# Kernel optimization log

Hardware: AMD Instinct MI355X
Metric: run time of the kernel (lower is better)

Reference implementation:

```python
import jax, jax.numpy as jnp
import numpy as np

E = 16        # n_routed_experts
K = 2         # n_activated_experts (top-k)
DIM = 1024    # model dim
INTER = 704   # moe_inter_dim
B, S = 4, 1024


def setup_inputs() -> dict:
    key = jax.random.key(0)
    ks = jax.random.split(key, 5)
    x = jax.random.normal(ks[0], (B, S, DIM), dtype=jnp.float32)
    Wg = jax.random.normal(ks[1], (E, DIM), dtype=jnp.float32) * 0.02   # gate (Linear, no bias)
    W1 = jax.random.normal(ks[2], (E, DIM, INTER), dtype=jnp.float32) * 0.02
    W3 = jax.random.normal(ks[3], (E, DIM, INTER), dtype=jnp.float32) * 0.02
    W2 = jax.random.normal(ks[4], (E, INTER, DIM), dtype=jnp.float32) * 0.02
    return {"x": x, "Wg": Wg, "W1": W1, "W2": W2, "W3": W3}


def reference(x, Wg, W1, W2, W3):
    # Single-process semantics of MoEWithAll2All: the all2all dispatch/combine is
    # pure communication; the math is: softmax router -> top-k -> renormalize ->
    # per-expert SwiGLU MLP on routed tokens -> weighted combine at original slots.
    Bb, Ss, D = x.shape
    xf = x.reshape(-1, D)                              # [N, D], N = B*S
    logits = xf @ Wg.T                                 # [N, E]
    probs = jax.nn.softmax(logits, axis=-1)
    topw, topi = jax.lax.top_k(probs, K)               # [N, K]
    topw = topw / topw.sum(axis=-1, keepdims=True)
    # gates[n, e] = routed weight of token n for expert e (0 if not routed):
    # identical math to the masked gather/scatter dispatch in the original.
    gates = (jax.nn.one_hot(topi, E, dtype=xf.dtype) * topw[..., None]).sum(axis=1)  # [N, E]
    out = jnp.zeros_like(xf)
    for e in range(E):                                 # small fixed loop over experts
        h = jax.nn.silu(xf @ W1[e]) * (xf @ W3[e])     # SwiGLU expert, [N, INTER]
        out = out + gates[:, e:e + 1] * (h @ W2[e])    # combine with gate weights
    return out.reshape(Bb, Ss, D)
```

## Files before the change

### kernel.cpp

```cpp
#include <hip/hip_runtime.h>

#define NTOK 4096
#define DDIM 1024
#define IDIM 704
#define NEXP 16
#define NSLOT 8192
#define MAXT 128
#define RTRBLK 512

typedef __attribute__((ext_vector_type(8))) short bf16x8;
typedef __attribute__((ext_vector_type(4))) float f32x4;
typedef __attribute__((ext_vector_type(4))) unsigned short us4;
typedef __attribute__((ext_vector_type(2))) unsigned int u32x2;

__device__ __forceinline__ unsigned short f2bf(float f) {
  union { float f; unsigned int u; } v; v.f = f;
  unsigned int r = v.u + 0x7fffu + ((v.u >> 16) & 1u);
  return (unsigned short)(r >> 16);
}

__device__ __forceinline__ float bf2f(unsigned short b) {
  union { unsigned int u; float f; } v; v.u = ((unsigned int)b) << 16;
  return v.f;
}

__device__ __forceinline__ unsigned int cvt_pk_bf16(float a, float b) {
  unsigned int r;
  asm("v_cvt_pk_bf16_f32 %0, %1, %2" : "=v"(r) : "v"(a), "v"(b));
  return r;
}

__device__ __forceinline__ void gload_lds16(const void* g, void* l) {
  __builtin_amdgcn_global_load_lds((const __attribute__((address_space(1))) void*)g,
                                   (__attribute__((address_space(3))) void*)l, 16, 0, 0);
}

__device__ __forceinline__ void load_b(const float* wt, int ns, bool ok, f32x4* v) {
#pragma unroll
  for (int j = 0; j < 4; ++j)
    v[j] = ok ? *(const f32x4*)(wt + (size_t)j * ns) : (f32x4)0.f;
}

__device__ __forceinline__ void write_b(const f32x4* v, unsigned short* buf, int kk, int nq) {
  int h8 = (kk & 1) * 8;
  int phys = (kk >> 1) ^ (nq & 3);
#pragma unroll
  for (int c = 0; c < 4; ++c) {
    int row = nq * 4 + c;
    u32x2 o = { cvt_pk_bf16(v[0][c], v[1][c]), cvt_pk_bf16(v[2][c], v[3][c]) };
    *(u32x2*)((char*)buf + row * 64 + phys * 16 + h8) = o;
  }
}

__global__ __launch_bounds__(256, 4)
void k_front(const float* __restrict__ x, const float* __restrict__ Wg,
             int* __restrict__ tok_e, float* __restrict__ tok_w,
             unsigned short* __restrict__ Xb) {
  int b = blockIdx.x;
  int lane = threadIdx.x & 63;
  int wv = threadIdx.x >> 6;
  int tk0 = b * 8 + wv * 2;
  f32x4 xv[2][4];
#pragma unroll
  for (int tok = 0; tok < 2; ++tok) {
    const f32x4* xr = (const f32x4*)(x + (size_t)(tk0 + tok) * DDIM);
    us4* xbr = (us4*)(Xb + (size_t)(tk0 + tok) * DDIM);
#pragma unroll
    for (int c = 0; c < 4; ++c) {
      xv[tok][c] = xr[c * 64 + lane];
      us4 o;
#pragma unroll
      for (int j = 0; j < 4; ++j) o[j] = f2bf(xv[tok][c][j]);
      xbr[c * 64 + lane] = o;
    }
  }
  float p[2][NEXP];
#pragma unroll
  for (int e = 0; e < NEXP; ++e) {
    const f32x4* wr = (const f32x4*)(Wg + (size_t)e * DDIM);
    float s0 = 0.f, s1 = 0.f;
#pragma unroll
    for (int c = 0; c < 4; ++c) {
      f32x4 w4 = wr[c * 64 + lane];
      s0 += xv[0][c][0]*w4[0] + xv[0][c][1]*w4[1] + xv[0][c][2]*w4[2] + xv[0][c][3]*w4[3];
      s1 += xv[1][c][0]*w4[0] + xv[1][c][1]*w4[1] + xv[1][c][2]*w4[2] + xv[1][c][3]*w4[3];
    }
    p[0][e] = s0; p[1][e] = s1;
  }
#pragma unroll
  for (int off = 32; off >= 1; off >>= 1)
#pragma unroll
    for (int e = 0; e < NEXP; ++e) {
      p[0][e] += __shfl_xor(p[0][e], off);
      p[1][e] += __shfl_xor(p[1][e], off);
    }
#pragma unroll
  for (int tok = 0; tok < 2; ++tok) {
    int i0 = 0; float b0 = p[tok][0];
#pragma unroll
    for (int e = 1; e < NEXP; ++e) if (p[tok][e] > b0) { b0 = p[tok][e]; i0 = e; }
    int i1 = -1; float b1 = -3.4e38f;
#pragma unroll
    for (int e = 0; e < NEXP; ++e) if (e != i0 && p[tok][e] > b1) { b1 = p[tok][e]; i1 = e; }
    if (lane == 0) {
      int tk = tk0 + tok;
      float w0 = 1.f / (1.f + __expf(b1 - b0));
      tok_e[2*tk] = i0; tok_e[2*tk+1] = i1;
      tok_w[2*tk] = w0; tok_w[2*tk+1] = 1.f - w0;
    }
  }
}

__global__ void k_scan_scatter(const int* __restrict__ tok_e, const float* __restrict__ tok_w,
                               int* __restrict__ counts, int* __restrict__ offsets,
                               int* __restrict__ ntiles, int* __restrict__ tile_e,
                               int* __restrict__ tile_m0, int* __restrict__ token_map,
                               float* __restrict__ gate_w, int* __restrict__ slot_of) {
  int eb = blockIdx.x;
  int t = threadIdx.x, lane = t & 63, wv = t >> 6;
  __shared__ unsigned long long masks[4][32];
  __shared__ int wcnt[4][NEXP];
  __shared__ int counts_s[NEXP];
  int ce[NEXP];
#pragma unroll
  for (int e = 0; e < NEXP; ++e) ce[e] = 0;
  int base = wv * 2048 + lane;
  int te = tok_e[base];
#pragma unroll 1
  for (int s = 0; s < 32; ++s) {
    int ten = (s < 31) ? tok_e[base + (s + 1) * 64] : 0;
    unsigned long long B0 = __ballot(te & 1);
    unsigned long long B1 = __ballot(te & 2);
    unsigned long long B2 = __ballot(te & 4);
    unsigned long long B3 = __ballot(te & 8);
#pragma unroll
    for (int e = 0; e < NEXP; ++e) {
      unsigned long long m = ((e & 1) ? B0 : ~B0) & ((e & 2) ? B1 : ~B1) &
                             ((e & 4) ? B2 : ~B2) & ((e & 8) ? B3 : ~B3);
      ce[e] += (int)__popcll(m);
      if (e == eb && lane == 0) masks[wv][s] = m;
    }
    te = ten;
  }
  if (lane == 0) {
#pragma unroll
    for (int e = 0; e < NEXP; ++e) wcnt[wv][e] = ce[e];
  }
  __syncthreads();
  if (t < NEXP) {
    int s = wcnt[0][t] + wcnt[1][t] + wcnt[2][t] + wcnt[3][t];
    counts_s[t] = s;
    if (eb == 0) counts[t] = s;
  }
  __syncthreads();
  if (eb == 0 && t == 0) {
    int acc = 0, nt = 0;
    for (int e = 0; e < NEXP; ++e) {
      offsets[e] = acc;
      int cc = counts_s[e];
      for (int m0 = 0; m0 < cc; m0 += 128) { tile_e[nt] = e; tile_m0[nt] = m0; ++nt; }
      acc += cc;
    }
    offsets[NEXP] = acc;
    *ntiles = nt;
  }
  int run = 0;
  for (int e = 0; e < eb; ++e) run += counts_s[e];
  for (int w = 0; w < wv; ++w) run += wcnt[w][eb];
  unsigned long long below = (lane == 63) ? 0x7fffffffffffffffull : ((1ull << lane) - 1ull);
#pragma unroll 1
  for (int s = 0; s < 32; ++s) {
    unsigned long long m = masks[wv][s];
    if ((m >> lane) & 1ull) {
      int i = wv * 2048 + s * 64 + lane;
      int slot = run + (int)__popcll(m & below);
      token_map[slot] = i >> 1;
      gate_w[slot] = tok_w[i];
      slot_of[i] = slot;
    }
    run += (int)__popcll(m);
  }
}

__global__ __launch_bounds__(256, 2)
void k_gemm1(const unsigned short* __restrict__ Xb, const float* __restrict__ W1,
             const float* __restrict__ W3, const int* __restrict__ token_map,
             const float* __restrict__ gate_w, const int* __restrict__ ntiles,
             const int* __restrict__ tile_e, const int* __restrict__ tile_m0,
             const int* __restrict__ offsets, const int* __restrict__ counts,
             unsigned short* __restrict__ H) {
  int idx = blockIdx.x;
  int xcd = idx & 7, r = idx >> 3;
  int g = (r >> 2) * 8 + xcd;
  int mm = r & 3;
  int ty = (g / 6) * 4 + mm;
  if (ty >= *ntiles) return;
  int n0 = (g % 6) * 128;
  int e = tile_e[ty], m0 = tile_m0[ty];
  int base_slot = offsets[e] + m0;
  int cnt = counts[e] - m0; if (cnt > 128) cnt = 128;

  __shared__ unsigned short As[2][128 * 32];
  __shared__ unsigned short B1s[2][128 * 32];
  __shared__ unsigned short B3s[2][128 * 32];

  int t = threadIdx.x;
  int arow = t >> 2, kc = (t & 3) * 8;
  int r0i = base_slot + arow;      if (r0i > NSLOT - 1) r0i = NSLOT - 1;
  int r1i = base_slot + 64 + arow; if (r1i > NSLOT - 1) r1i = NSLOT - 1;
  const unsigned short* ag0 = Xb + (size_t)token_map[r0i] * DDIM + kc;
  const unsigned short* ag1 = Xb + (size_t)token_map[r1i] * DDIM + kc;
  int d0 = t * 8, d1 = 2048 + t * 8;

  int kk = t >> 5, nq = t & 31;
  bool bok = (n0 + nq * 4 + 4) <= IDIM;
  const float* w1t = W1 + (size_t)e * DDIM * IDIM + (size_t)(kk * 4) * IDIM + (n0 + nq * 4);
  const float* w3t = W3 + (size_t)e * DDIM * IDIM + (size_t)(kk * 4) * IDIM + (n0 + nq * 4);

  int lane = t & 63, wv = t >> 6;
  int wm = (wv >> 1) * 64, wn = (wv & 1) * 64;
  int lm = lane & 15, kg = lane >> 4;
  int ao[4], bo[4];
#pragma unroll
  for (int i = 0; i < 4; ++i) {
    ao[i] = (wm + i * 16 + lm) * 32 + kg * 8;
    int brow = wn + i * 16 + lm;
    bo[i] = brow * 64 + ((kg ^ ((brow >> 2) & 3)) << 4);
  }

  f32x4 acc1[4][4], acc3[4][4];
#pragma unroll
  for (int i = 0; i < 4; ++i)
#pragma unroll
    for (int j = 0; j < 4; ++j) { acc1[i][j] = 0.f; acc3[i][j] = 0.f; }

  {
    gload_lds16(ag0, As[0] + d0);
    gload_lds16(ag1, As[0] + d1);
    f32x4 b1r[4], b3r[4];
    load_b(w1t, IDIM, bok, b1r);
    load_b(w3t, IDIM, bok, b3r);
    write_b(b1r, B1s[0], kk, nq);
    write_b(b3r, B3s[0], kk, nq);
  }

  for (int k0 = 0; k0 < DDIM; k0 += 32) {
    int cur = (k0 >> 5) & 1, nx = cur ^ 1;
    __syncthreads();
    f32x4 b1r[4], b3r[4];
    bool more = (k0 + 32) < DDIM;
    if (more) {
      int kn = k0 + 32;
      gload_lds16(ag0 + kn, As[nx] + d0);
      gload_lds16(ag1 + kn, As[nx] + d1);
      load_b(w1t + (size_t)kn * IDIM, IDIM, bok, b1r);
      load_b(w3t + (size_t)kn * IDIM, IDIM, bok, b3r);
    }
    bf16x8 av[4], b1v[4], b3v[4];
#pragma unroll
    for (int i = 0; i < 4; ++i) {
      av[i]  = *(const bf16x8*)(As[cur] + ao[i]);
      b1v[i] = *(const bf16x8*)((const char*)B1s[cur] + bo[i]);
      b3v[i] = *(const bf16x8*)((const char*)B3s[cur] + bo[i]);
    }
#pragma unroll
    for (int mi = 0; mi < 4; ++mi)
#pragma unroll
      for (int ni = 0; ni < 4; ++ni) {
        acc1[mi][ni] = __builtin_amdgcn_mfma_f32_16x16x32_bf16(av[mi], b1v[ni], acc1[mi][ni], 0, 0, 0);
        acc3[mi][ni] = __builtin_amdgcn_mfma_f32_16x16x32_bf16(av[mi], b3v[ni], acc3[mi][ni], 0, 0, 0);
      }
    if (more) {
      write_b(b1r, B1s[nx], kk, nq);
      write_b(b3r, B3s[nx], kk, nq);
    }
  }

#pragma unroll
  for (int mi = 0; mi < 4; ++mi)
#pragma unroll
    for (int rr = 0; rr < 4; ++rr) {
      int orow = wm + mi * 16 + kg * 4 + rr;
      if (orow < cnt) {
        int slot = base_slot + orow;
        float gw = gate_w[slot];
        unsigned short* hrow = H + (size_t)slot * IDIM;
#pragma unroll
        for (int ni = 0; ni < 4; ++ni) {
          int nn = n0 + wn + ni * 16 + lm;
          if (nn < IDIM) {
            float v1 = acc1[mi][ni][rr];
            float v3 = acc3[mi][ni][rr];
            float hh = v1 / (1.f + __expf(-v1)) * v3 * gw;
            hrow[nn] = f2bf(hh);
          }
        }
      }
    }
}

__global__ __launch_bounds__(256, 3)
void k_gemm2(const unsigned short* __restrict__ H, const float* __restrict__ W2,
             const int* __restrict__ ntiles, const int* __restrict__ tile_e,
             const int* __restrict__ tile_m0, const int* __restrict__ offsets,
             const int* __restrict__ counts, unsigned short* __restrict__ O2) {
  int idx = blockIdx.x;
  int xcd = idx & 7, r = idx >> 3;
  int g = (r >> 2) * 8 + xcd;
  int mm = r & 3;
  int ty = (g >> 3) * 4 + mm;
  if (ty >= *ntiles) return;
  int n0 = (g & 7) * 128;
  int e = tile_e[ty], m0 = tile_m0[ty];
  int base_slot = offsets[e] + m0;
  int cnt = counts[e] - m0; if (cnt > 128) cnt = 128;

  __shared__ unsigned short As[2][128 * 32];
  __shared__ unsigned short Bs[2][128 * 32];

  int t = threadIdx.x;
  int arow = t >> 2, kc = (t & 3) * 8;
  int r0i = base_slot + arow;      if (r0i > NSLOT - 1) r0i = NSLOT - 1;
  int r1i = base_slot + 64 + arow; if (r1i > NSLOT - 1) r1i = NSLOT - 1;
  const unsigned short* ag0 = H + (size_t)r0i * IDIM + kc;
  const unsigned short* ag1 = H + (size_t)r1i * IDIM + kc;
  int d0 = t * 8, d1 = 2048 + t * 8;

  int kk = t >> 5, nq = t & 31;
  const float* w2t = W2 + (size_t)e * IDIM * DDIM + (size_t)(kk * 4) * DDIM + (n0 + nq * 4);

  int lane = t & 63, wv = t >> 6;
  int wm = (wv >> 1) * 64, wn = (wv & 1) * 64;
  int lm = lane & 15, kg = lane >> 4;
  int ao[4], bo[4];
#pragma unroll
  for (int i = 0; i < 4; ++i) {
    ao[i] = (wm + i * 16 + lm) * 32 + kg * 8;
    int brow = wn + i * 16 + lm;
    bo[i] = brow * 64 + ((kg ^ ((brow >> 2) & 3)) << 4);
  }

  f32x4 acc[4][4];
#pragma unroll
  for (int i = 0; i < 4; ++i)
#pragma unroll
    for (int j = 0; j < 4; ++j) acc[i][j] = 0.f;

  {
    gload_lds16(ag0, As[0] + d0);
    gload_lds16(ag1, As[0] + d1);
    f32x4 br[4];
    load_b(w2t, DDIM, true, br);
    write_b(br, Bs[0], kk, nq);
  }

  for (int k0 = 0; k0 < IDIM; k0 += 32) {
    int cur = (k0 >> 5) & 1, nx = cur ^ 1;
    __syncthreads();
    f32x4 br[4];
    bool more = (k0 + 32) < IDIM;
    if (more) {
      int kn = k0 + 32;
      gload_lds16(ag0 + kn, As[nx] + d0);
      gload_lds16(ag1 + kn, As[nx] + d1);
      load_b(w2t + (size_t)kn * DDIM, DDIM, true, br);
    }
    bf16x8 av[4], bv[4];
#pragma unroll
    for (int i = 0; i < 4; ++i) {
      av[i] = *(const bf16x8*)(As[cur] + ao[i]);
      bv[i] = *(const bf16x8*)((const char*)Bs[cur] + bo[i]);
    }
#pragma unroll
    for (int mi = 0; mi < 4; ++mi)
#pragma unroll
      for (int ni = 0; ni < 4; ++ni)
        acc[mi][ni] = __builtin_amdgcn_mfma_f32_16x16x32_bf16(av[mi], bv[ni], acc[mi][ni], 0, 0, 0);
    if (more) write_b(br, Bs[nx], kk, nq);
  }

#pragma unroll
  for (int mi = 0; mi < 4; ++mi)
#pragma unroll
    for (int rr = 0; rr < 4; ++rr) {
      int orow = wm + mi * 16 + kg * 4 + rr;
      if (orow < cnt) {
        unsigned short* op = O2 + (size_t)(base_slot + orow) * DDIM + n0;
#pragma unroll
        for (int ni = 0; ni < 4; ++ni)
          op[wn + ni * 16 + lm] = f2bf(acc[mi][ni][rr]);
      }
    }
}

__global__ void k_combine(const unsigned short* __restrict__ O2, const int* __restrict__ slot_of,
                          float* __restrict__ out) {
  int tk = blockIdx.x, tt = threadIdx.x;
  int s0 = slot_of[2 * tk], s1 = slot_of[2 * tk + 1];
  us4 a = ((const us4*)(O2 + (size_t)s0 * DDIM))[tt];
  us4 b = ((const us4*)(O2 + (size_t)s1 * DDIM))[tt];
  f32x4 o;
#pragma unroll
  for (int j = 0; j < 4; ++j) o[j] = bf2f(a[j]) + bf2f(b[j]);
  ((f32x4*)(out + (size_t)tk * DDIM))[tt] = o;
}

extern "C" void kernel_launch(void* const* d_in, const int* in_sizes, int n_in,
                              void* d_out, int out_size, void* d_ws, size_t ws_size,
                              hipStream_t stream) {
  const float* x  = (const float*)d_in[0];
  const float* Wg = (const float*)d_in[1];
  const float* W1 = (const float*)d_in[2];
  const float* W2 = (const float*)d_in[3];
  const float* W3 = (const float*)d_in[4];
  float* out = (float*)d_out;

  char* ws = (char*)d_ws;
  size_t off = 0;
  unsigned short* Xb = (unsigned short*)(ws + off); off += (size_t)NTOK * DDIM * 2;
  unsigned short* H  = (unsigned short*)(ws + off); off += (size_t)NSLOT * IDIM * 2;
  unsigned short* O2 = (unsigned short*)(ws + off); off += (size_t)NSLOT * DDIM * 2;
  int* counts  = (int*)(ws + off); off += 64;
  int* offsets = (int*)(ws + off); off += 128;
  int* ntiles  = (int*)(ws + off); off += 64;
  int* tile_e  = (int*)(ws + off); off += MAXT * 4;
  int* tile_m0 = (int*)(ws + off); off += MAXT * 4;
  int* tok_e   = (int*)(ws + off); off += NSLOT * 4;
  float* tok_w = (float*)(ws + off); off += NSLOT * 4;
  int* token_map = (int*)(ws + off); off += NSLOT * 4;
  float* gate_w  = (float*)(ws + off); off += NSLOT * 4;
  int* slot_of   = (int*)(ws + off); off += NSLOT * 4;

  k_front<<<RTRBLK, 256, 0, stream>>>(x, Wg, tok_e, tok_w, Xb);
  k_scan_scatter<<<NEXP, 256, 0, stream>>>(tok_e, tok_w, counts, offsets, ntiles,
                                           tile_e, tile_m0, token_map, gate_w, slot_of);
  k_gemm1<<<480, 256, 0, stream>>>(Xb, W1, W3, token_map, gate_w, ntiles, tile_e,
                                   tile_m0, offsets, counts, H);
  k_gemm2<<<640, 256, 0, stream>>>(H, W2, ntiles, tile_e, tile_m0, offsets, counts, O2);
  k_combine<<<4096, 256, 0, stream>>>(O2, slot_of, out);
}
```

Measured before the change: 318.3 us.

## Halve GEMM N-tile to 64 and split weight loading across thread halves

Both expert GEMMs switch from 128x128 to 128x64 output tiles, with each wave taking a 32-row strip. This roughly doubles the grid (880 and 1280 blocks) and raises the occupancy hints. In gemm1, half the threads load W1 and the other half W3, which removes the per-thread dual weight load and the bounds check, since 704 is a multiple of 64. The B-tile LDS writes also rotate their column order per thread to reduce bank conflicts. The trade-off is that the A tile is reloaded for twice as many N-tiles, raising gathered activation traffic, and only half the threads load weights in gemm2.

```diff
diff --git a/kernel.cpp b/kernel.cpp
--- a/kernel.cpp
+++ b/kernel.cpp
@@ -35,17 +35,18 @@
                                    (__attribute__((address_space(3))) void*)l, 16, 0, 0);
 }
 
-__device__ __forceinline__ void load_b(const float* wt, int ns, bool ok, f32x4* v) {
+__device__ __forceinline__ void load_b(const float* wt, int ns, f32x4* v) {
 #pragma unroll
   for (int j = 0; j < 4; ++j)
-    v[j] = ok ? *(const f32x4*)(wt + (size_t)j * ns) : (f32x4)0.f;
+    v[j] = *(const f32x4*)(wt + (size_t)j * ns);
 }
 
 __device__ __forceinline__ void write_b(const f32x4* v, unsigned short* buf, int kk, int nq) {
   int h8 = (kk & 1) * 8;
-  int phys = (kk >> 1) ^ (nq & 3);
-#pragma unroll
-  for (int c = 0; c < 4; ++c) {
+  int phys = ((kk >> 1) ^ nq) & 3;
+#pragma unroll
+  for (int cc = 0; cc < 4; ++cc) {
+    int c = (cc + nq) & 3;
     int row = nq * 4 + c;
     u32x2 o = { cvt_pk_bf16(v[0][c], v[1][c]), cvt_pk_bf16(v[2][c], v[3][c]) };
     *(u32x2*)((char*)buf + row * 64 + phys * 16 + h8) = o;
@@ -182,27 +183,25 @@
   }
 }
 
-__global__ __launch_bounds__(256, 2)
+__global__ __launch_bounds__(256, 3)
 void k_gemm1(const unsigned short* __restrict__ Xb, const float* __restrict__ W1,
              const float* __restrict__ W3, const int* __restrict__ token_map,
              const float* __restrict__ gate_w, const int* __restrict__ ntiles,
              const int* __restrict__ tile_e, const int* __restrict__ tile_m0,
              const int* __restrict__ offsets, const int* __restrict__ counts,
              unsigned short* __restrict__ H) {
-  int idx = blockIdx.x;
-  int xcd = idx & 7, r = idx >> 3;
-  int g = (r >> 2) * 8 + xcd;
-  int mm = r & 3;
-  int ty = (g / 6) * 4 + mm;
+  int wg = blockIdx.x;
+  int g = (wg & 7) * 110 + (wg >> 3);
+  int ty = g / 11, nb = g % 11;
   if (ty >= *ntiles) return;
-  int n0 = (g % 6) * 128;
+  int n0 = nb * 64;
   int e = tile_e[ty], m0 = tile_m0[ty];
   int base_slot = offsets[e] + m0;
   int cnt = counts[e] - m0; if (cnt > 128) cnt = 128;
 
   __shared__ unsigned short As[2][128 * 32];
-  __shared__ unsigned short B1s[2][128 * 32];
-  __shared__ unsigned short B3s[2][128 * 32];
+  __shared__ unsigned short B1s[2][64 * 32];
+  __shared__ unsigned short B3s[2][64 * 32];
 
   int t = threadIdx.x;
   int arow = t >> 2, kc = (t & 3) * 8;
@@ -212,111 +211,103 @@
   const unsigned short* ag1 = Xb + (size_t)token_map[r1i] * DDIM + kc;
   int d0 = t * 8, d1 = 2048 + t * 8;
 
-  int kk = t >> 5, nq = t & 31;
-  bool bok = (n0 + nq * 4 + 4) <= IDIM;
-  const float* w1t = W1 + (size_t)e * DDIM * IDIM + (size_t)(kk * 4) * IDIM + (n0 + nq * 4);
-  const float* w3t = W3 + (size_t)e * DDIM * IDIM + (size_t)(kk * 4) * IDIM + (n0 + nq * 4);
+  int bmat = t >> 7;
+  int bt = t & 127;
+  int nq = bt & 15, kk = bt >> 4;
+  const float* wsrc = (bmat ? W3 : W1) + (size_t)e * DDIM * IDIM
+                      + (size_t)(kk * 4) * IDIM + (n0 + nq * 4);
+  unsigned short (*Bst)[64 * 32] = bmat ? B3s : B1s;
 
   int lane = t & 63, wv = t >> 6;
-  int wm = (wv >> 1) * 64, wn = (wv & 1) * 64;
+  int wm = wv * 32;
   int lm = lane & 15, kg = lane >> 4;
-  int ao[4], bo[4];
+  int ao[2], bo[4];
+#pragma unroll
+  for (int i = 0; i < 2; ++i) ao[i] = (wm + i * 16 + lm) * 32 + kg * 8;
 #pragma unroll
   for (int i = 0; i < 4; ++i) {
-    ao[i] = (wm + i * 16 + lm) * 32 + kg * 8;
-    int brow = wn + i * 16 + lm;
+    int brow = i * 16 + lm;
     bo[i] = brow * 64 + ((kg ^ ((brow >> 2) & 3)) << 4);
   }
 
-  f32x4 acc1[4][4], acc3[4][4];
-#pragma unroll
-  for (int i = 0; i < 4; ++i)
+  f32x4 acc1[2][4], acc3[2][4];
+#pragma unroll
+  for (int i = 0; i < 2; ++i)
 #pragma unroll
     for (int j = 0; j < 4; ++j) { acc1[i][j] = 0.f; acc3[i][j] = 0.f; }
 
+  f32x4 br[4];
   {
     gload_lds16(ag0, As[0] + d0);
     gload_lds16(ag1, As[0] + d1);
-    f32x4 b1r[4], b3r[4];
-    load_b(w1t, IDIM, bok, b1r);
-    load_b(w3t, IDIM, bok, b3r);
-    write_b(b1r, B1s[0], kk, nq);
-    write_b(b3r, B3s[0], kk, nq);
+    load_b(wsrc, IDIM, br);
+    write_b(br, Bst[0], kk, nq);
   }
 
   for (int k0 = 0; k0 < DDIM; k0 += 32) {
     int cur = (k0 >> 5) & 1, nx = cur ^ 1;
     __syncthreads();
-    f32x4 b1r[4], b3r[4];
     bool more = (k0 + 32) < DDIM;
     if (more) {
       int kn = k0 + 32;
       gload_lds16(ag0 + kn, As[nx] + d0);
       gload_lds16(ag1 + kn, As[nx] + d1);
-      load_b(w1t + (size_t)kn * IDIM, IDIM, bok, b1r);
-      load_b(w3t + (size_t)kn * IDIM, IDIM, bok, b3r);
-    }
-    bf16x8 av[4], b1v[4], b3v[4];
+      load_b(wsrc + (size_t)kn * IDIM, IDIM, br);
+    }
+    bf16x8 av[2], b1v[4], b3v[4];
+#pragma unroll
+    for (int i = 0; i < 2; ++i) av[i] = *(const bf16x8*)(As[cur] + ao[i]);
 #pragma unroll
     for (int i = 0; i < 4; ++i) {
-      av[i]  = *(const bf16x8*)(As[cur] + ao[i]);
       b1v[i] = *(const bf16x8*)((const char*)B1s[cur] + bo[i]);
       b3v[i] = *(const bf16x8*)((const char*)B3s[cur] + bo[i]);
     }
 #pragma unroll
-    for (int mi = 0; mi < 4; ++mi)
+    for (int mi = 0; mi < 2; ++mi)
 #pragma unroll
       for (int ni = 0; ni < 4; ++ni) {
         acc1[mi][ni] = __builtin_amdgcn_mfma_f32_16x16x32_bf16(av[mi], b1v[ni], acc1[mi][ni], 0, 0, 0);
         acc3[mi][ni] = __builtin_amdgcn_mfma_f32_16x16x32_bf16(av[mi], b3v[ni], acc3[mi][ni], 0, 0, 0);
       }
-    if (more) {
-      write_b(b1r, B1s[nx], kk, nq);
-      write_b(b3r, B3s[nx], kk, nq);
-    }
-  }
-
-#pragma unroll
-  for (int mi = 0; mi < 4; ++mi)
+    if (more) write_b(br, Bst[nx], kk, nq);
+  }
+
+#pragma unroll
+  for (int mi = 0; mi < 2; ++mi)
 #pragma unroll
     for (int rr = 0; rr < 4; ++rr) {
       int orow = wm + mi * 16 + kg * 4 + rr;
       if (orow < cnt) {
         int slot = base_slot + orow;
         float gw = gate_w[slot];
-        unsigned short* hrow = H + (size_t)slot * IDIM;
+        unsigned short* hrow = H + (size_t)slot * IDIM + n0;
 #pragma unroll
         for (int ni = 0; ni < 4; ++ni) {
-          int nn = n0 + wn + ni * 16 + lm;
-          if (nn < IDIM) {
-            float v1 = acc1[mi][ni][rr];
-            float v3 = acc3[mi][ni][rr];
-            float hh = v1 / (1.f + __expf(-v1)) * v3 * gw;
-            hrow[nn] = f2bf(hh);
-          }
+          float v1 = acc1[mi][ni][rr];
+          float v3 = acc3[mi][ni][rr];
+          float hh = v1 / (1.f + __expf(-v1)) * v3 * gw;
+          hrow[ni * 16 + lm] = f2bf(hh);
         }
       }
     }
 }
 
-__global__ __launch_bounds__(256, 3)
+__global__ __launch_bounds__(256, 4)
 void k_gemm2(const unsigned short* __restrict__ H, const float* __restrict__ W2,
              const int* __restrict__ ntiles, const int* __restrict__ tile_e,
              const int* __restrict__ tile_m0, const int* __restrict__ offsets,
              const int* __restrict__ counts, unsigned short* __restrict__ O2) {
-  int idx = blockIdx.x;
-  int xcd = idx & 7, r = idx >> 3;
-  int g = (r >> 2) * 8 + xcd;
-  int mm = r & 3;
-  int ty = (g >> 3) * 4 + mm;
+  int wg = blockIdx.x;
+  int g = (wg & 7) * 160 + (wg >> 3);
+  int ty = g >> 4, nb = g & 15;
   if (ty >= *ntiles) return;
-  int n0 = (g & 7) * 128;
+  int n0 = nb * 64;
   int e = tile_e[ty], m0 = tile_m0[ty];
   int base_slot = offsets[e] + m0;
   int cnt = counts[e] - m0; if (cnt > 128) cnt = 128;
 
   __shared__ unsigned short As[2][128 * 32];
-  __shared__ unsigned short Bs[2][128 * 32];
+  __shared__ unsigned short Bs[2][64 * 32];
 
   int t = threadIdx.x;
   int arow = t >> 2, kc = (t & 3) * 8;
@@ -326,61 +317,63 @@
   const unsigned short* ag1 = H + (size_t)r1i * IDIM + kc;
   int d0 = t * 8, d1 = 2048 + t * 8;
 
-  int kk = t >> 5, nq = t & 31;
-  const float* w2t = W2 + (size_t)e * IDIM * DDIM + (size_t)(kk * 4) * DDIM + (n0 + nq * 4);
+  int bt = t & 127;
+  int nq = bt & 15, kk = bt >> 4;
+  const float* wsrc = W2 + (size_t)e * IDIM * DDIM + (size_t)(kk * 4) * DDIM + (n0 + nq * 4);
 
   int lane = t & 63, wv = t >> 6;
-  int wm = (wv >> 1) * 64, wn = (wv & 1) * 64;
+  int wm = wv * 32;
   int lm = lane & 15, kg = lane >> 4;
-  int ao[4], bo[4];
+  int ao[2], bo[4];
+#pragma unroll
+  for (int i = 0; i < 2; ++i) ao[i] = (wm + i * 16 + lm) * 32 + kg * 8;
 #pragma unroll
   for (int i = 0; i < 4; ++i) {
-    ao[i] = (wm + i * 16 + lm) * 32 + kg * 8;
-    int brow = wn + i * 16 + lm;
+    int brow = i * 16 + lm;
     bo[i] = brow * 64 + ((kg ^ ((brow >> 2) & 3)) << 4);
   }
 
-  f32x4 acc[4][4];
-#pragma unroll
-  for (int i = 0; i < 4; ++i)
+  f32x4 acc[2][4];
+#pragma unroll
+  for (int i = 0; i < 2; ++i)
 #pragma unroll
     for (int j = 0; j < 4; ++j) acc[i][j] = 0.f;
 
+  f32x4 br[4];
   {
     gload_lds16(ag0, As[0] + d0);
     gload_lds16(ag1, As[0] + d1);
-    f32x4 br[4];
-    load_b(w2t, DDIM, true, br);
-    write_b(br, Bs[0], kk, nq);
+    if (t < 128) {
+      load_b(wsrc, DDIM, br);
+      write_b(br, Bs[0], kk, nq);
+    }
   }
 
   for (int k0 = 0; k0 < IDIM; k0 += 32) {
     int cur = (k0 >> 5) & 1, nx = cur ^ 1;
     __syncthreads();
-    f32x4 br[4];
     bool more = (k0 + 32) < IDIM;
     if (more) {
       int kn = k0 + 32;
       gload_lds16(ag0 + kn, As[nx] + d0);
       gload_lds16(ag1 + kn, As[nx] + d1);
-      load_b(w2t + (size_t)kn * DDIM, DDIM, true, br);
-    }
-    bf16x8 av[4], bv[4];
-#pragma unroll
-    for (int i = 0; i < 4; ++i) {
-      av[i] = *(const bf16x8*)(As[cur] + ao[i]);
-      bv[i] = *(const bf16x8*)((const char*)Bs[cur] + bo[i]);
-    }
-#pragma unroll
-    for (int mi = 0; mi < 4; ++mi)
+      if (t < 128) load_b(wsrc + (size_t)kn * DDIM, DDIM, br);
+    }
+    bf16x8 av[2], bv[4];
+#pragma unroll
+    for (int i = 0; i < 2; ++i) av[i] = *(const bf16x8*)(As[cur] + ao[i]);
+#pragma unroll
+    for (int i = 0; i < 4; ++i) bv[i] = *(const bf16x8*)((const char*)Bs[cur] + bo[i]);
+#pragma unroll
+    for (int mi = 0; mi < 2; ++mi)
 #pragma unroll
       for (int ni = 0; ni < 4; ++ni)
         acc[mi][ni] = __builtin_amdgcn_mfma_f32_16x16x32_bf16(av[mi], bv[ni], acc[mi][ni], 0, 0, 0);
-    if (more) write_b(br, Bs[nx], kk, nq);
-  }
-
-#pragma unroll
-  for (int mi = 0; mi < 4; ++mi)
+    if (more && t < 128) write_b(br, Bs[nx], kk, nq);
+  }
+
+#pragma unroll
+  for (int mi = 0; mi < 2; ++mi)
 #pragma unroll
     for (int rr = 0; rr < 4; ++rr) {
       int orow = wm + mi * 16 + kg * 4 + rr;
@@ -388,7 +381,7 @@
         unsigned short* op = O2 + (size_t)(base_slot + orow) * DDIM + n0;
 #pragma unroll
         for (int ni = 0; ni < 4; ++ni)
-          op[wn + ni * 16 + lm] = f2bf(acc[mi][ni][rr]);
+          op[ni * 16 + lm] = f2bf(acc[mi][ni][rr]);
       }
     }
 }
@@ -434,8 +427,8 @@
   k_front<<<RTRBLK, 256, 0, stream>>>(x, Wg, tok_e, tok_w, Xb);
   k_scan_scatter<<<NEXP, 256, 0, stream>>>(tok_e, tok_w, counts, offsets, ntiles,
                                            tile_e, tile_m0, token_map, gate_w, slot_of);
-  k_gemm1<<<480, 256, 0, stream>>>(Xb, W1, W3, token_map, gate_w, ntiles, tile_e,
+  k_gemm1<<<880, 256, 0, stream>>>(Xb, W1, W3, token_map, gate_w, ntiles, tile_e,
                                    tile_m0, offsets, counts, H);
-  k_gemm2<<<640, 256, 0, stream>>>(H, W2, ntiles, tile_e, tile_m0, offsets, counts, O2);
+  k_gemm2<<<1280, 256, 0, stream>>>(H, W2, ntiles, tile_e, tile_m0, offsets, counts, O2);
   k_combine<<<4096, 256, 0, stream>>>(O2, slot_of, out);
 }
```

Measured after the change: 488.5 us. 1.53x slower.

## Pre-transpose W2 to bf16 inside gemm1 grid and use direct LDS loads in gemm2

Applied to the files above, without the earlier changes.

Adds extra blocks to the gemm1 launch that convert W2 from fp32 [I,D] to a bf16 transposed [D,I] workspace buffer through a swizzled LDS tile. gemm2 then loads its B operand with global_load_lds like the A operand, dropping the per-iteration fp32 register loads, conversion and LDS writes. It also rotates the store order in write_b to reduce LDS bank conflicts. The cost is an extra full pass over W2 (read fp32, write bf16) each call, which adds work to the gemm1 launch and consumes bandwidth alongside it.

```diff
diff --git a/kernel.cpp b/kernel.cpp
--- a/kernel.cpp
+++ b/kernel.cpp
@@ -7,10 +7,13 @@
 #define NSLOT 8192
 #define MAXT 128
 #define RTRBLK 512
+#define G1BLK 480
+#define W2TBLK 1408
 
 typedef __attribute__((ext_vector_type(8))) short bf16x8;
 typedef __attribute__((ext_vector_type(4))) float f32x4;
 typedef __attribute__((ext_vector_type(4))) unsigned short us4;
+typedef __attribute__((ext_vector_type(8))) unsigned short us8;
 typedef __attribute__((ext_vector_type(2))) unsigned int u32x2;
 
 __device__ __forceinline__ unsigned short f2bf(float f) {
@@ -45,7 +48,8 @@
   int h8 = (kk & 1) * 8;
   int phys = (kk >> 1) ^ (nq & 3);
 #pragma unroll
-  for (int c = 0; c < 4; ++c) {
+  for (int cc = 0; cc < 4; ++cc) {
+    int c = (cc + nq) & 3;
     int row = nq * 4 + c;
     u32x2 o = { cvt_pk_bf16(v[0][c], v[1][c]), cvt_pk_bf16(v[2][c], v[3][c]) };
     *(u32x2*)((char*)buf + row * 64 + phys * 16 + h8) = o;
@@ -184,12 +188,55 @@
 
 __global__ __launch_bounds__(256, 2)
 void k_gemm1(const unsigned short* __restrict__ Xb, const float* __restrict__ W1,
-             const float* __restrict__ W3, const int* __restrict__ token_map,
-             const float* __restrict__ gate_w, const int* __restrict__ ntiles,
-             const int* __restrict__ tile_e, const int* __restrict__ tile_m0,
-             const int* __restrict__ offsets, const int* __restrict__ counts,
-             unsigned short* __restrict__ H) {
+             const float* __restrict__ W3, const float* __restrict__ W2src,
+             const int* __restrict__ token_map, const float* __restrict__ gate_w,
+             const int* __restrict__ ntiles, const int* __restrict__ tile_e,
+             const int* __restrict__ tile_m0, const int* __restrict__ offsets,
+             const int* __restrict__ counts, unsigned short* __restrict__ H,
+             unsigned short* __restrict__ W2T) {
+  __shared__ unsigned short As[2][128 * 32];
+  __shared__ unsigned short B1s[2][128 * 32];
+  __shared__ unsigned short B3s[2][128 * 32];
   int idx = blockIdx.x;
+  int t = threadIdx.x;
+  if (idx >= G1BLK) {
+    unsigned short (*lds)[64 * 64] = (unsigned short (*)[64 * 64])As;
+    int tb = idx - G1BLK;
+    int kx = tb % 11; int rest = tb / 11; int np = rest & 7; int e = rest >> 3;
+    const float* src = W2src + (size_t)e * IDIM * DDIM;
+    unsigned short* dst = W2T + (size_t)e * DDIM * IDIM;
+    int k0 = kx * 64;
+    int kr4 = (t >> 4) * 4, nc4 = (t & 15) * 4;
+    int n0a = np * 128, n0b = n0a + 64;
+    f32x4 v0[4], v1[4];
+#pragma unroll
+    for (int j = 0; j < 4; ++j) {
+      v0[j] = *(const f32x4*)(src + (size_t)(k0 + kr4 + j) * DDIM + n0a + nc4);
+      v1[j] = *(const f32x4*)(src + (size_t)(k0 + kr4 + j) * DDIM + n0b + nc4);
+    }
+    int c8 = kr4 >> 3, half = (kr4 >> 2) & 1;
+#pragma unroll
+    for (int i = 0; i < 4; ++i) {
+      int row = nc4 + i;
+      int addr = row * 64 + ((c8 ^ ((row >> 2) & 7)) << 3) + half * 4;
+      us4 o0 = { f2bf(v0[0][i]), f2bf(v0[1][i]), f2bf(v0[2][i]), f2bf(v0[3][i]) };
+      us4 o1 = { f2bf(v1[0][i]), f2bf(v1[1][i]), f2bf(v1[2][i]), f2bf(v1[3][i]) };
+      *(us4*)(lds[0] + addr) = o0;
+      *(us4*)(lds[1] + addr) = o1;
+    }
+    __syncthreads();
+    int nr = t >> 3, kc8 = t & 7;
+#pragma unroll
+    for (int q = 0; q < 2; ++q) {
+      int row = nr + q * 32;
+      int a = row * 64 + ((kc8 ^ ((row >> 2) & 7)) << 3);
+      us8 oA = *(const us8*)(lds[0] + a);
+      us8 oB = *(const us8*)(lds[1] + a);
+      *(us8*)(dst + (size_t)(n0a + row) * IDIM + k0 + kc8 * 8) = oA;
+      *(us8*)(dst + (size_t)(n0b + row) * IDIM + k0 + kc8 * 8) = oB;
+    }
+    return;
+  }
   int xcd = idx & 7, r = idx >> 3;
   int g = (r >> 2) * 8 + xcd;
   int mm = r & 3;
@@ -200,11 +247,6 @@
   int base_slot = offsets[e] + m0;
   int cnt = counts[e] - m0; if (cnt > 128) cnt = 128;
 
-  __shared__ unsigned short As[2][128 * 32];
-  __shared__ unsigned short B1s[2][128 * 32];
-  __shared__ unsigned short B3s[2][128 * 32];
-
-  int t = threadIdx.x;
   int arow = t >> 2, kc = (t & 3) * 8;
   int r0i = base_slot + arow;      if (r0i > NSLOT - 1) r0i = NSLOT - 1;
   int r1i = base_slot + 64 + arow; if (r1i > NSLOT - 1) r1i = NSLOT - 1;
@@ -300,7 +342,7 @@
 }
 
 __global__ __launch_bounds__(256, 3)
-void k_gemm2(const unsigned short* __restrict__ H, const float* __restrict__ W2,
+void k_gemm2(const unsigned short* __restrict__ H, const unsigned short* __restrict__ W2T,
              const int* __restrict__ ntiles, const int* __restrict__ tile_e,
              const int* __restrict__ tile_m0, const int* __restrict__ offsets,
              const int* __restrict__ counts, unsigned short* __restrict__ O2) {
@@ -319,15 +361,14 @@
   __shared__ unsigned short Bs[2][128 * 32];
 
   int t = threadIdx.x;
-  int arow = t >> 2, kc = (t & 3) * 8;
-  int r0i = base_slot + arow;      if (r0i > NSLOT - 1) r0i = NSLOT - 1;
-  int r1i = base_slot + 64 + arow; if (r1i > NSLOT - 1) r1i = NSLOT - 1;
+  int row = t >> 2, kc = (t & 3) * 8;
+  int r0i = base_slot + row;      if (r0i > NSLOT - 1) r0i = NSLOT - 1;
+  int r1i = base_slot + 64 + row; if (r1i > NSLOT - 1) r1i = NSLOT - 1;
   const unsigned short* ag0 = H + (size_t)r0i * IDIM + kc;
   const unsigned short* ag1 = H + (size_t)r1i * IDIM + kc;
+  const unsigned short* bg0 = W2T + ((size_t)e * DDIM + n0 + row) * IDIM + kc;
+  const unsigned short* bg1 = bg0 + (size_t)64 * IDIM;
   int d0 = t * 8, d1 = 2048 + t * 8;
-
-  int kk = t >> 5, nq = t & 31;
-  const float* w2t = W2 + (size_t)e * IDIM * DDIM + (size_t)(kk * 4) * DDIM + (n0 + nq * 4);
 
   int lane = t & 63, wv = t >> 6;
   int wm = (wv >> 1) * 64, wn = (wv & 1) * 64;
@@ -336,8 +377,7 @@
 #pragma unroll
   for (int i = 0; i < 4; ++i) {
     ao[i] = (wm + i * 16 + lm) * 32 + kg * 8;
-    int brow = wn + i * 16 + lm;
-    bo[i] = brow * 64 + ((kg ^ ((brow >> 2) & 3)) << 4);
+    bo[i] = (wn + i * 16 + lm) * 32 + kg * 8;
   }
 
   f32x4 acc[4][4];
@@ -346,37 +386,32 @@
 #pragma unroll
     for (int j = 0; j < 4; ++j) acc[i][j] = 0.f;
 
-  {
-    gload_lds16(ag0, As[0] + d0);
-    gload_lds16(ag1, As[0] + d1);
-    f32x4 br[4];
-    load_b(w2t, DDIM, true, br);
-    write_b(br, Bs[0], kk, nq);
-  }
+  gload_lds16(ag0, As[0] + d0);
+  gload_lds16(ag1, As[0] + d1);
+  gload_lds16(bg0, Bs[0] + d0);
+  gload_lds16(bg1, Bs[0] + d1);
 
   for (int k0 = 0; k0 < IDIM; k0 += 32) {
-    int cur = (k0 >> 5) & 1, nx = cur ^ 1;
+    int cur = (k0 >> 5) & 1;
     __syncthreads();
-    f32x4 br[4];
-    bool more = (k0 + 32) < IDIM;
-    if (more) {
-      int kn = k0 + 32;
+    if (k0 + 32 < IDIM) {
+      int nx = cur ^ 1, kn = k0 + 32;
       gload_lds16(ag0 + kn, As[nx] + d0);
       gload_lds16(ag1 + kn, As[nx] + d1);
-      load_b(w2t + (size_t)kn * DDIM, DDIM, true, br);
+      gload_lds16(bg0 + kn, Bs[nx] + d0);
+      gload_lds16(bg1 + kn, Bs[nx] + d1);
     }
     bf16x8 av[4], bv[4];
 #pragma unroll
     for (int i = 0; i < 4; ++i) {
       av[i] = *(const bf16x8*)(As[cur] + ao[i]);
-      bv[i] = *(const bf16x8*)((const char*)Bs[cur] + bo[i]);
+      bv[i] = *(const bf16x8*)(Bs[cur] + bo[i]);
     }
 #pragma unroll
     for (int mi = 0; mi < 4; ++mi)
 #pragma unroll
       for (int ni = 0; ni < 4; ++ni)
         acc[mi][ni] = __builtin_amdgcn_mfma_f32_16x16x32_bf16(av[mi], bv[ni], acc[mi][ni], 0, 0, 0);
-    if (more) write_b(br, Bs[nx], kk, nq);
   }
 
 #pragma unroll
@@ -420,6 +455,7 @@
   unsigned short* Xb = (unsigned short*)(ws + off); off += (size_t)NTOK * DDIM * 2;
   unsigned short* H  = (unsigned short*)(ws + off); off += (size_t)NSLOT * IDIM * 2;
   unsigned short* O2 = (unsigned short*)(ws + off); off += (size_t)NSLOT * DDIM * 2;
+  unsigned short* W2T = (unsigned short*)(ws + off); off += (size_t)NEXP * DDIM * IDIM * 2;
   int* counts  = (int*)(ws + off); off += 64;
   int* offsets = (int*)(ws + off); off += 128;
   int* ntiles  = (int*)(ws + off); off += 64;
@@ -434,8 +470,9 @@
   k_front<<<RTRBLK, 256, 0, stream>>>(x, Wg, tok_e, tok_w, Xb);
   k_scan_scatter<<<NEXP, 256, 0, stream>>>(tok_e, tok_w, counts, offsets, ntiles,
                                            tile_e, tile_m0, token_map, gate_w, slot_of);
-  k_gemm1<<<480, 256, 0, stream>>>(Xb, W1, W3, token_map, gate_w, ntiles, tile_e,
-                                   tile_m0, offsets, counts, H);
-  k_gemm2<<<640, 256, 0, stream>>>(H, W2, ntiles, tile_e, tile_m0, offsets, counts, O2);
+  k_gemm1<<<G1BLK + W2TBLK, 256, 0, stream>>>(Xb, W1, W3, W2, token_map, gate_w,
+                                              ntiles, tile_e, tile_m0, offsets, counts,
+                                              H, W2T);
+  k_gemm2<<<640, 256, 0, stream>>>(H, W2T, ntiles, tile_e, tile_m0, offsets, counts, O2);
   k_combine<<<4096, 256, 0, stream>>>(O2, slot_of, out);
 }
```

Result: slower. 376.8 us (+18.4%).

## Deepen weight prefetch to two stages and rotate LDS write order to cut bank conflicts

Applied to the files above, without the earlier changes.

Both expert GEMM kernels now prefetch the fp32 weight tile two k-steps ahead into registers. The register tile from the previous iteration is written to LDS at the start of each iteration, before the MFMA block, so global-load latency has a full iteration to hide. The write_b helper also rotates the row order per thread group and masks the swizzle, which spreads LDS stores across banks. This keeps weight registers live across the loop, which raises register pressure and may reduce occupancy under launch_bounds(256,4).

```diff
diff --git a/kernel.cpp b/kernel.cpp
--- a/kernel.cpp
+++ b/kernel.cpp
@@ -43,9 +43,10 @@
 
 __device__ __forceinline__ void write_b(const f32x4* v, unsigned short* buf, int kk, int nq) {
   int h8 = (kk & 1) * 8;
-  int phys = (kk >> 1) ^ (nq & 3);
-#pragma unroll
-  for (int c = 0; c < 4; ++c) {
+  int phys = ((kk >> 1) ^ nq) & 3;
+#pragma unroll
+  for (int cc = 0; cc < 4; ++cc) {
+    int c = (cc + (nq >> 2)) & 3;
     int row = nq * 4 + c;
     u32x2 o = { cvt_pk_bf16(v[0][c], v[1][c]), cvt_pk_bf16(v[2][c], v[3][c]) };
     *(u32x2*)((char*)buf + row * 64 + phys * 16 + h8) = o;
@@ -234,27 +235,32 @@
 #pragma unroll
     for (int j = 0; j < 4; ++j) { acc1[i][j] = 0.f; acc3[i][j] = 0.f; }
 
+  f32x4 b1r[4], b3r[4];
   {
     gload_lds16(ag0, As[0] + d0);
     gload_lds16(ag1, As[0] + d1);
-    f32x4 b1r[4], b3r[4];
     load_b(w1t, IDIM, bok, b1r);
     load_b(w3t, IDIM, bok, b3r);
     write_b(b1r, B1s[0], kk, nq);
     write_b(b3r, B3s[0], kk, nq);
-  }
-
-  for (int k0 = 0; k0 < DDIM; k0 += 32) {
-    int cur = (k0 >> 5) & 1, nx = cur ^ 1;
+    load_b(w1t + (size_t)32 * IDIM, IDIM, bok, b1r);
+    load_b(w3t + (size_t)32 * IDIM, IDIM, bok, b3r);
+  }
+
+  for (int ks = 0; ks < 32; ++ks) {
+    int cur = ks & 1, nx = cur ^ 1;
     __syncthreads();
-    f32x4 b1r[4], b3r[4];
-    bool more = (k0 + 32) < DDIM;
-    if (more) {
-      int kn = k0 + 32;
+    if (ks + 1 < 32) {
+      write_b(b1r, B1s[nx], kk, nq);
+      write_b(b3r, B3s[nx], kk, nq);
+      int kn = (ks + 1) * 32;
       gload_lds16(ag0 + kn, As[nx] + d0);
       gload_lds16(ag1 + kn, As[nx] + d1);
-      load_b(w1t + (size_t)kn * IDIM, IDIM, bok, b1r);
-      load_b(w3t + (size_t)kn * IDIM, IDIM, bok, b3r);
+      if (ks + 2 < 32) {
+        int k2 = (ks + 2) * 32;
+        load_b(w1t + (size_t)k2 * IDIM, IDIM, bok, b1r);
+        load_b(w3t + (size_t)k2 * IDIM, IDIM, bok, b3r);
+      }
     }
     bf16x8 av[4], b1v[4], b3v[4];
 #pragma unroll
@@ -270,10 +276,6 @@
         acc1[mi][ni] = __builtin_amdgcn_mfma_f32_16x16x32_bf16(av[mi], b1v[ni], acc1[mi][ni], 0, 0, 0);
         acc3[mi][ni] = __builtin_amdgcn_mfma_f32_16x16x32_bf16(av[mi], b3v[ni], acc3[mi][ni], 0, 0, 0);
       }
-    if (more) {
-      write_b(b1r, B1s[nx], kk, nq);
-      write_b(b3r, B3s[nx], kk, nq);
-    }
   }
 
 #pragma unroll
@@ -346,24 +348,27 @@
 #pragma unroll
     for (int j = 0; j < 4; ++j) acc[i][j] = 0.f;
 
+  const int NK = IDIM / 32;
+  f32x4 br[4];
   {
     gload_lds16(ag0, As[0] + d0);
     gload_lds16(ag1, As[0] + d1);
-    f32x4 br[4];
     load_b(w2t, DDIM, true, br);
     write_b(br, Bs[0], kk, nq);
-  }
-
-  for (int k0 = 0; k0 < IDIM; k0 += 32) {
-    int cur = (k0 >> 5) & 1, nx = cur ^ 1;
+    load_b(w2t + (size_t)32 * DDIM, DDIM, true, br);
+  }
+
+  for (int ks = 0; ks < NK; ++ks) {
+    int cur = ks & 1, nx = cur ^ 1;
     __syncthreads();
-    f32x4 br[4];
-    bool more = (k0 + 32) < IDIM;
-    if (more) {
-      int kn = k0 + 32;
+    if (ks + 1 < NK) {
+      write_b(br, Bs[nx], kk, nq);
+      int kn = (ks + 1) * 32;
       gload_lds16(ag0 + kn, As[nx] + d0);
       gload_lds16(ag1 + kn, As[nx] + d1);
-      load_b(w2t + (size_t)kn * DDIM, DDIM, true, br);
+      if (ks + 2 < NK) {
+        load_b(w2t + (size_t)((ks + 2) * 32) * DDIM, DDIM, true, br);
+      }
     }
     bf16x8 av[4], bv[4];
 #pragma unroll
@@ -376,7 +381,6 @@
 #pragma unroll
       for (int ni = 0; ni < 4; ++ni)
         acc[mi][ni] = __builtin_amdgcn_mfma_f32_16x16x32_bf16(av[mi], bv[ni], acc[mi][ni], 0, 0, 0);
-    if (more) write_b(br, Bs[nx], kk, nq);
   }
 
 #pragma unroll
```

Result: slower. 437.8 us (+37.5%).
